# Kernel tuning notes

Measured on AMD Instinct MI355X. Metric: run time of the kernel, lower is better.

Reference implementation:

```python
import jax, jax.numpy as jnp
import numpy as np

B, NPG, EPG = 512, 256, 4096   # graphs, nodes/graph, edges/graph
N, E = B * NPG, B * EPG
F_IN, H, T = 128, 64, 18
K = 16
D_LAT = 4 * H + 1  # 257


def _p(key, shape, scale=0.05):
    return jax.random.normal(key, shape, dtype=jnp.float32) * scale


def setup_inputs() -> dict:
    key = jax.random.key(0)
    ks = jax.random.split(key, 32)
    x = jax.random.normal(ks[0], (N, F_IN), dtype=jnp.float32)
    off = jnp.repeat(jnp.arange(B, dtype=jnp.int32) * NPG, EPG)
    src = jax.random.randint(ks[1], (E,), 0, NPG, dtype=jnp.int32) + off
    dst = jax.random.randint(ks[2], (E,), 0, NPG, dtype=jnp.int32) + off
    edge_index = jnp.stack([src, dst])
    batch = jnp.repeat(jnp.arange(B, dtype=jnp.int32), NPG)
    inp = {"x": x, "edge_index": edge_index, "batch": batch, "num_graphs": B}
    dims = [F_IN, H, H, H, H]
    outs = [H, H, H, H, 1]
    for i in range(5):
        inp[f"w{i}"] = _p(ks[3 + i], (outs[i], dims[i]))
        inp[f"b{i}"] = jnp.zeros((outs[i],), jnp.float32)
    inp["conv1_w"] = _p(ks[10], (16, 1, D_LAT))
    inp["conv1_b"] = jnp.zeros((16,), jnp.float32)
    inp["conv2_w"] = _p(ks[11], (32, 16, 5))
    inp["conv2_b"] = jnp.zeros((32,), jnp.float32)
    inp["d1_w"] = _p(ks[12], (32, 128))
    inp["d1_b"] = jnp.zeros((32,), jnp.float32)
    inp["d2_w"] = _p(ks[13], (T, 32))
    inp["d2_b"] = jnp.zeros((T,), jnp.float32)
    return inp


def _dgcnn_forward(x, edge_index, batch, num_graphs,
                   ws, bs, conv1_w, conv1_b, conv2_w, conv2_b,
                   d1_w, d1_b, d2_w, d2_b):
    n_nodes = x.shape[0]
    loops = jnp.arange(n_nodes, dtype=edge_index.dtype)
    src = jnp.concatenate([edge_index[0], loops])
    dst = jnp.concatenate([edge_index[1], loops])
    # degree of src indices (with self-loops), norm = 1/deg gathered at dst
    deg = jax.ops.segment_sum(jnp.ones_like(src, x.dtype), src, num_segments=n_nodes)
    inv_deg_dst = (1.0 / deg)[dst]  # deg >= 1 thanks to self-loops

    hidden = []
    h = x
    for w, b in zip(ws, bs):
        h = h @ w.T + b                       # linear transform [N, out]
        msg = h[src] * inv_deg_dst[:, None]    # gather + degree norm [E+N, out]
        h = jax.ops.segment_sum(msg, dst, num_segments=n_nodes)
        h = jnp.tanh(h)
        hidden.append(h)
    feat = jnp.concatenate(hidden, axis=1)     # [N, 257]

    # global_sort_pool: per-graph descending sort on last channel, take top-k
    npg = n_nodes // num_graphs
    xr = feat.reshape(num_graphs, npg, D_LAT)
    order = jnp.argsort(-xr[:, :, -1], axis=1)[:, :K]         # [B, K]
    topk = jnp.take_along_axis(xr, order[:, :, None], axis=1)  # [B, K, 257]

    # conv1d(1->16, kernel=stride=257) over flattened [B, K*257] == per-slot matmul
    c1 = jnp.einsum('bld,od->bol', topk, conv1_w[:, 0, :]) + conv1_b[None, :, None]
    c1 = jax.nn.relu(c1)                                       # [B, 16, 16]
    p1 = c1.reshape(num_graphs, 16, K // 2, 2).max(axis=-1)    # maxpool1d(2,2) -> [B,16,8]
    c2 = jax.lax.conv_general_dilated(p1, conv2_w, (1,), 'VALID',
                                      dimension_numbers=('NCH', 'OIH', 'NCH'))
    c2 = jax.nn.relu(c2 + conv2_b[None, :, None])              # [B, 32, 4]
    flat = c2.reshape(num_graphs, -1)                          # [B, 128]
    last = jax.nn.relu(flat @ d1_w.T + d1_b)                   # [B, 32]
    out = last @ d2_w.T + d2_b                                 # [B, T] (dropout: eval mode)
    return jax.nn.log_softmax(out, axis=1), out, last


def reference(x, edge_index, batch, num_graphs,
              w0, b0, w1, b1, w2, b2, w3, b3, w4, b4,
              conv1_w, conv1_b, conv2_w, conv2_b,
              d1_w, d1_b, d2_w, d2_b):
    ws = [w0, w1, w2, w3, w4]
    bs = [b0, b1, b2, b3, b4]
    return _dgcnn_forward(x, edge_index, batch, num_graphs, ws, bs,
                          conv1_w, conv1_b, conv2_w, conv2_b,
                          d1_w, d1_b, d2_w, d2_b)
```

## Files before the change

kernel.cpp:

```cpp
#include <hip/hip_runtime.h>
#include <math.h>

#define NPG  256
#define EPG  4096
#define NG   512
#define FIN  128
#define HD   64
#define TOUT 18
#define KTOP 16
#define STB  260
#define STA  68
#define SRCL_CAP (EPG + 3*NPG)
#define E_TOT (NG*EPG)

__device__ __forceinline__ int HB(int k) { return k*STB + (((k>>2)&7)<<2); }

__launch_bounds__(1024)
__global__ void dgcnn_fused(
    const float* __restrict__ x,
    const int*   __restrict__ ei,
    const float* __restrict__ w0, const float* __restrict__ b0,
    const float* __restrict__ w1, const float* __restrict__ b1,
    const float* __restrict__ w2, const float* __restrict__ b2,
    const float* __restrict__ w3, const float* __restrict__ b3,
    const float* __restrict__ w4, const float* __restrict__ b4,
    const float* __restrict__ c1w, const float* __restrict__ c1b,
    const float* __restrict__ c2w, const float* __restrict__ c2b,
    const float* __restrict__ d1w, const float* __restrict__ d1b,
    const float* __restrict__ d2w, const float* __restrict__ d2b,
    float* __restrict__ out)
{
    __shared__ float s_hB[HD*STB + 32];
    __shared__ float s_hl[NPG*STA];
    __shared__ unsigned char s_srcl[SRCL_CAP] __attribute__((aligned(4)));
    __shared__ int   s_off[NPG+1];
    __shared__ int   s_cnt[NPG];
    __shared__ int   s_outd[NPG];
    __shared__ int   s_cur[NPG];
    __shared__ float s_invdeg[NPG];
    __shared__ float s_lin5[NPG];
    __shared__ float s_h5[NPG];
    __shared__ int   s_sel[KTOP];
    __shared__ float s_head[592];

    const int g = blockIdx.x;
    const int t = threadIdx.x;
    const int lane = t & 63;
    const int wid  = t >> 6;
    const int l4 = lane * 4;
    const int gbase = g * NPG;
    const int* __restrict__ srcg = ei + (size_t)g * EPG;
    const int* __restrict__ dstg = ei + (size_t)E_TOT + (size_t)g * EPG;

    if (t < NPG) { s_cnt[t] = 0; s_outd[t] = 0; }
    __syncthreads();
    for (int e = t; e < EPG; e += 1024) {
        int s = srcg[e] - gbase, d = dstg[e] - gbase;
        atomicAdd(&s_outd[s], 1);
        atomicAdd(&s_cnt[d], 1);
    }
    __syncthreads();
    if (t < NPG) s_invdeg[t] = 1.0f / (float)(s_outd[t] + 1);
    if (wid == 0) {
        int c0 = s_cnt[l4], c1 = s_cnt[l4+1], c2 = s_cnt[l4+2], c3 = s_cnt[l4+3];
        int p0 = (c0+3)&~3, p1 = (c1+3)&~3, p2 = (c2+3)&~3, p3 = (c3+3)&~3;
        int tot = p0+p1+p2+p3;
        int run = tot;
        #pragma unroll
        for (int o = 1; o < 64; o <<= 1) {
            int v = __shfl_up(run, o);
            if (lane >= o) run += v;
        }
        int base = run - tot;
        s_off[l4]   = base;
        s_off[l4+1] = base + p0;
        s_off[l4+2] = base + p0 + p1;
        s_off[l4+3] = base + p0 + p1 + p2;
        if (lane == 63) s_off[NPG] = run;
    }
    __syncthreads();
    if (t < NPG) s_cur[t] = s_off[t];
    __syncthreads();
    for (int e = t; e < EPG; e += 1024) {
        int s = srcg[e] - gbase, d = dstg[e] - gbase;
        int pos = atomicAdd(&s_cur[d], 1);
        s_srcl[pos] = (unsigned char)s;
    }
    __syncthreads();
    if (t < NPG) {
        int pe = s_off[t+1];
        for (int p = s_cur[t]; p < pe; p++) s_srcl[p] = (unsigned char)t;
    }
    __syncthreads();

    float projacc[4][4];
    #pragma unroll
    for (int i = 0; i < 4; i++)
        #pragma unroll
        for (int j = 0; j < 4; j++) projacc[i][j] = 0.f;

    auto aggregate = [&]() {
        const int js = lane >> 4;
        const int q4 = (lane & 15) * 4;
        for (int job = wid; job < 64; job += 16) {
            int d   = job*4 + js;
            int off = s_off[d], pe = s_off[d+1];
            int npad = (pe - off) - s_cnt[d];
            float4 a = *(const float4*)&s_hl[d*STA + (q4 ^ (((d>>2)&7)<<2))];
            float cf = (float)(1 - npad);
            a.x *= cf; a.y *= cf; a.z *= cf; a.w *= cf;
            for (int e = off; e < pe; e += 4) {
                unsigned int sq = *(const unsigned int*)&s_srcl[e];
                #pragma unroll
                for (int m = 0; m < 4; m++) {
                    int src = (sq >> (8*m)) & 255;
                    float4 hv = *(const float4*)&s_hl[src*STA + (q4 ^ (((src>>2)&7)<<2))];
                    a.x += hv.x; a.y += hv.y; a.z += hv.z; a.w += hv.w;
                }
            }
            float id = s_invdeg[d];
            s_hB[HB(q4+0) + d] = tanhf(a.x * id);
            s_hB[HB(q4+1) + d] = tanhf(a.y * id);
            s_hB[HB(q4+2) + d] = tanhf(a.z * id);
            s_hB[HB(q4+3) + d] = tanhf(a.w * id);
        }
    };

    auto matmul64 = [&](const float* __restrict__ w, const float* __restrict__ b) {
        const int c0 = __builtin_amdgcn_readfirstlane(wid * 4);
        const float* wp = w + c0 * HD;
        float acc[4][4];
        #pragma unroll
        for (int i = 0; i < 4; i++)
            #pragma unroll
            for (int j = 0; j < 4; j++) acc[i][j] = 0.f;
        #pragma unroll 8
        for (int k = 0; k < HD; k++) {
            float4 xv = *(const float4*)&s_hB[HB(k) + l4];
            float wv0 = wp[k], wv1 = wp[HD+k], wv2 = wp[2*HD+k], wv3 = wp[3*HD+k];
            float xa[4] = {xv.x, xv.y, xv.z, xv.w};
            #pragma unroll
            for (int i = 0; i < 4; i++) {
                acc[i][0] += xa[i]*wv0; acc[i][1] += xa[i]*wv1;
                acc[i][2] += xa[i]*wv2; acc[i][3] += xa[i]*wv3;
            }
        }
        float4 bb = *(const float4*)&b[c0];
        float ba[4] = {bb.x, bb.y, bb.z, bb.w};
        int colb = (wid*4) ^ ((lane & 7) << 2);
        #pragma unroll
        for (int i = 0; i < 4; i++) {
            float4 v;
            v.x = acc[i][0]+ba[0]; v.y = acc[i][1]+ba[1];
            v.z = acc[i][2]+ba[2]; v.w = acc[i][3]+ba[3];
            *(float4*)&s_hl[(l4+i)*STA + colb] = v;
        }
    };

    auto projpass = [&](int Loff) {
        const int o0 = __builtin_amdgcn_readfirstlane(wid * 4);
        const float* p = c1w + o0*257 + Loff;
        #pragma unroll 8
        for (int k = 0; k < HD; k++) {
            float4 xv = *(const float4*)&s_hB[HB(k) + l4];
            float p0 = p[k], p1 = p[257+k], p2 = p[514+k], p3 = p[771+k];
            float xa[4] = {xv.x, xv.y, xv.z, xv.w};
            #pragma unroll
            for (int i = 0; i < 4; i++) {
                projacc[i][0] += xa[i]*p0; projacc[i][1] += xa[i]*p1;
                projacc[i][2] += xa[i]*p2; projacc[i][3] += xa[i]*p3;
            }
        }
    };

    {
        const int c0 = __builtin_amdgcn_readfirstlane(wid * 4);
        float acc[4][4];
        #pragma unroll
        for (int i = 0; i < 4; i++)
            #pragma unroll
            for (int j = 0; j < 4; j++) acc[i][j] = 0.f;
        for (int c2 = 0; c2 < 2; c2++) {
            {
                int kk = (t & 15) * 4, nb = t >> 4;
                #pragma unroll
                for (int r = 0; r < 4; r++) {
                    int nn = nb + r*64;
                    float4 v = *(const float4*)&x[(size_t)(gbase+nn)*FIN + c2*64 + kk];
                    s_hB[HB(kk+0) + nn] = v.x;
                    s_hB[HB(kk+1) + nn] = v.y;
                    s_hB[HB(kk+2) + nn] = v.z;
                    s_hB[HB(kk+3) + nn] = v.w;
                }
            }
            __syncthreads();
            const float* wp = w0 + c0*FIN + c2*64;
            #pragma unroll 8
            for (int k = 0; k < 64; k++) {
                float4 xv = *(const float4*)&s_hB[HB(k) + l4];
                float wv0 = wp[k], wv1 = wp[FIN+k], wv2 = wp[2*FIN+k], wv3 = wp[3*FIN+k];
                float xa[4] = {xv.x, xv.y, xv.z, xv.w};
                #pragma unroll
                for (int i = 0; i < 4; i++) {
                    acc[i][0] += xa[i]*wv0; acc[i][1] += xa[i]*wv1;
                    acc[i][2] += xa[i]*wv2; acc[i][3] += xa[i]*wv3;
                }
            }
            __syncthreads();
        }
        float4 bb = *(const float4*)&b0[c0];
        float ba[4] = {bb.x, bb.y, bb.z, bb.w};
        int colb = (wid*4) ^ ((lane & 7) << 2);
        #pragma unroll
        for (int i = 0; i < 4; i++) {
            float4 v;
            v.x = acc[i][0]+ba[0]; v.y = acc[i][1]+ba[1];
            v.z = acc[i][2]+ba[2]; v.w = acc[i][3]+ba[3];
            *(float4*)&s_hl[(l4+i)*STA + colb] = v;
        }
    }
    __syncthreads();
    aggregate();
    __syncthreads();

    if (wid < 4) projpass(0);
    matmul64(w1, b1);
    __syncthreads();
    aggregate();
    __syncthreads();

    if (wid < 4) projpass(64);
    matmul64(w2, b2);
    __syncthreads();
    aggregate();
    __syncthreads();

    if (wid < 4) projpass(128);
    matmul64(w3, b3);
    __syncthreads();
    aggregate();
    __syncthreads();

    if (wid < 4) {
        projpass(192);
    } else if (wid < 8) {
        int n = t - 256;
        float a = b4[0];
        #pragma unroll 8
        for (int k = 0; k < HD; k++) a += s_hB[HB(k) + n] * w4[k];
        s_lin5[n] = a;
    }
    __syncthreads();
    if (t < NPG) {
        int d = t;
        int off = s_off[d], pe = s_off[d+1];
        int npad = (pe - off) - s_cnt[d];
        float a = (float)(1 - npad) * s_lin5[d];
        for (int e = off; e < pe; e += 4) {
            unsigned int sq = *(const unsigned int*)&s_srcl[e];
            a += s_lin5[sq & 255] + s_lin5[(sq>>8)&255]
               + s_lin5[(sq>>16)&255] + s_lin5[(sq>>24)&255];
        }
        s_h5[d] = tanhf(a * s_invdeg[d]);
    }
    __syncthreads();
    if (wid < 4) {
        const int o0 = __builtin_amdgcn_readfirstlane(wid * 4);
        float cw0 = c1w[(o0+0)*257 + 256];
        float cw1 = c1w[(o0+1)*257 + 256];
        float cw2 = c1w[(o0+2)*257 + 256];
        float cw3 = c1w[(o0+3)*257 + 256];
        #pragma unroll
        for (int i = 0; i < 4; i++) {
            float hv = s_h5[l4+i];
            float4 v;
            v.x = projacc[i][0] + hv*cw0;
            v.y = projacc[i][1] + hv*cw1;
            v.z = projacc[i][2] + hv*cw2;
            v.w = projacc[i][3] + hv*cw3;
            *(float4*)&s_hl[(l4+i)*16 + wid*4] = v;
        }
    }
    if (wid == 0) {
        float v[4]; int idx[4];
        #pragma unroll
        for (int j = 0; j < 4; j++) { idx[j] = l4+j; v[j] = s_h5[l4+j]; }
        for (int r = 0; r < KTOP; r++) {
            float bv = v[0]; int bi = idx[0];
            #pragma unroll
            for (int j = 1; j < 4; j++)
                if (v[j] > bv || (v[j] == bv && idx[j] < bi)) { bv = v[j]; bi = idx[j]; }
            #pragma unroll
            for (int o = 32; o > 0; o >>= 1) {
                float ov = __shfl_xor(bv, o);
                int   oi = __shfl_xor(bi, o);
                if (ov > bv || (ov == bv && oi < bi)) { bv = ov; bi = oi; }
            }
            if ((bi >> 2) == lane) v[bi & 3] = -1e30f;
            if (lane == 0) s_sel[r] = bi;
        }
    }
    __syncthreads();

    float* s_c1   = s_head;
    float* s_p1   = s_head + 256;
    float* s_flat = s_head + 384;
    float* s_last = s_head + 512;
    float* s_outv = s_head + 544;

    if (t < 256) {
        int sl = t >> 4, o = t & 15;
        float vv = s_hl[s_sel[sl]*16 + o] + c1b[o];
        s_c1[o*16 + sl] = fmaxf(vv, 0.f);
    }
    __syncthreads();
    if (t < 128) {
        int o = t >> 3, j = t & 7;
        s_p1[o*8 + j] = fmaxf(s_c1[o*16 + 2*j], s_c1[o*16 + 2*j + 1]);
    }
    __syncthreads();
    if (t < 128) {
        int oc = t >> 2, tt = t & 3;
        float a = c2b[oc];
        #pragma unroll
        for (int ic = 0; ic < 16; ic++)
            #pragma unroll
            for (int kk = 0; kk < 5; kk++)
                a += s_p1[ic*8 + tt + kk] * c2w[(oc*16 + ic)*5 + kk];
        s_flat[oc*4 + tt] = fmaxf(a, 0.f);
    }
    __syncthreads();
    if (t < 32) {
        float a = d1b[t];
        #pragma unroll 16
        for (int i = 0; i < 128; i++) a += s_flat[i] * d1w[t*128 + i];
        a = fmaxf(a, 0.f);
        s_last[t] = a;
        out[2*NG*TOUT + g*32 + t] = a;
    }
    __syncthreads();
    if (t < TOUT) {
        float a = d2b[t];
        #pragma unroll
        for (int j = 0; j < 32; j++) a += s_last[j] * d2w[t*32 + j];
        s_outv[t] = a;
        out[NG*TOUT + g*TOUT + t] = a;
    }
    __syncthreads();
    if (t < TOUT) {
        float m = s_outv[0];
        for (int i = 1; i < TOUT; i++) m = fmaxf(m, s_outv[i]);
        float sum = 0.f;
        for (int i = 0; i < TOUT; i++) sum += expf(s_outv[i] - m);
        out[g*TOUT + t] = s_outv[t] - m - logf(sum);
    }
}

extern "C" void kernel_launch(void* const* d_in, const int* in_sizes, int n_in,
                              void* d_out, int out_size, void* d_ws, size_t ws_size,
                              hipStream_t stream) {
    (void)in_sizes; (void)n_in; (void)out_size; (void)d_ws; (void)ws_size;
    const float* x   = (const float*)d_in[0];
    const int*   ei  = (const int*)  d_in[1];
    const float* w0  = (const float*)d_in[4];  const float* b0 = (const float*)d_in[5];
    const float* w1  = (const float*)d_in[6];  const float* b1 = (const float*)d_in[7];
    const float* w2  = (const float*)d_in[8];  const float* b2 = (const float*)d_in[9];
    const float* w3  = (const float*)d_in[10]; const float* b3 = (const float*)d_in[11];
    const float* w4  = (const float*)d_in[12]; const float* b4 = (const float*)d_in[13];
    const float* c1w = (const float*)d_in[14]; const float* c1b = (const float*)d_in[15];
    const float* c2w = (const float*)d_in[16]; const float* c2b = (const float*)d_in[17];
    const float* d1w = (const float*)d_in[18]; const float* d1b = (const float*)d_in[19];
    const float* d2w = (const float*)d_in[20]; const float* d2b = (const float*)d_in[21];
    float* out = (float*)d_out;

    dgcnn_fused<<<NG, 1024, 0, stream>>>(x, ei,
        w0, b0, w1, b1, w2, b2, w3, b3, w4, b4,
        c1w, c1b, c2w, c2b, d1w, d1b, d2w, d2b, out);
}
```

Baseline: 174.4 us.

## Fuse conv1 projection into layer matmuls across all waves, prefetch edge lists

The separate projection pass for the conv1 weights, which only waves 0-3 ran with 4 output channels each, is removed. Every wave now carries one output channel of the projection and accumulates it inside the layer matmul loop, so the load imbalance before each barrier goes away. The aggregation loop is fully unrolled over its four jobs and software-prefetches the next packed source index word, which needs a small pad on the index buffer. The projection buffer uses stride 17, and launch bounds now ask for 4 waves per EU, which may raise register pressure or cause spills.

```diff
diff --git a/kernel.cpp b/kernel.cpp
--- a/kernel.cpp
+++ b/kernel.cpp
@@ -11,11 +11,12 @@
 #define STB  260
 #define STA  68
 #define SRCL_CAP (EPG + 3*NPG)
+#define SRCL_PAD (SRCL_CAP + 8)
 #define E_TOT (NG*EPG)
 
 __device__ __forceinline__ int HB(int k) { return k*STB + (((k>>2)&7)<<2); }
 
-__launch_bounds__(1024)
+__launch_bounds__(1024, 4)
 __global__ void dgcnn_fused(
     const float* __restrict__ x,
     const int*   __restrict__ ei,
@@ -32,7 +33,7 @@
 {
     __shared__ float s_hB[HD*STB + 32];
     __shared__ float s_hl[NPG*STA];
-    __shared__ unsigned char s_srcl[SRCL_CAP] __attribute__((aligned(4)));
+    __shared__ unsigned char s_srcl[SRCL_PAD] __attribute__((aligned(4)));
     __shared__ int   s_off[NPG+1];
     __shared__ int   s_cnt[NPG];
     __shared__ int   s_outd[NPG];
@@ -42,6 +43,7 @@
     __shared__ float s_h5[NPG];
     __shared__ int   s_sel[KTOP];
     __shared__ float s_head[592];
+    float* s_proj = s_hl;
 
     const int g = blockIdx.x;
     const int t = threadIdx.x;
@@ -93,30 +95,30 @@
     }
     __syncthreads();
 
-    float projacc[4][4];
-    #pragma unroll
-    for (int i = 0; i < 4; i++)
-        #pragma unroll
-        for (int j = 0; j < 4; j++) projacc[i][j] = 0.f;
+    float projacc[4] = {0.f, 0.f, 0.f, 0.f};
 
     auto aggregate = [&]() {
         const int js = lane >> 4;
         const int q4 = (lane & 15) * 4;
-        for (int job = wid; job < 64; job += 16) {
-            int d   = job*4 + js;
+        #pragma unroll
+        for (int r = 0; r < 4; r++) {
+            int d   = (wid + 16*r)*4 + js;
             int off = s_off[d], pe = s_off[d+1];
             int npad = (pe - off) - s_cnt[d];
             float4 a = *(const float4*)&s_hl[d*STA + (q4 ^ (((d>>2)&7)<<2))];
             float cf = (float)(1 - npad);
             a.x *= cf; a.y *= cf; a.z *= cf; a.w *= cf;
-            for (int e = off; e < pe; e += 4) {
-                unsigned int sq = *(const unsigned int*)&s_srcl[e];
+            unsigned int cur = *(const unsigned int*)&s_srcl[off];
+            for (int e = off; e < pe; ) {
+                e += 4;
+                unsigned int nxt = *(const unsigned int*)&s_srcl[e];
                 #pragma unroll
                 for (int m = 0; m < 4; m++) {
-                    int src = (sq >> (8*m)) & 255;
+                    int src = (cur >> (8*m)) & 255;
                     float4 hv = *(const float4*)&s_hl[src*STA + (q4 ^ (((src>>2)&7)<<2))];
                     a.x += hv.x; a.y += hv.y; a.z += hv.z; a.w += hv.w;
                 }
+                cur = nxt;
             }
             float id = s_invdeg[d];
             s_hB[HB(q4+0) + d] = tanhf(a.x * id);
@@ -126,9 +128,12 @@
         }
     };
 
-    auto matmul64 = [&](const float* __restrict__ w, const float* __restrict__ b) {
+    auto matmul64 = [&](const float* __restrict__ w, const float* __restrict__ b,
+                        const float* __restrict__ c1s) {
         const int c0 = __builtin_amdgcn_readfirstlane(wid * 4);
+        const int o  = __builtin_amdgcn_readfirstlane(wid);
         const float* wp = w + c0 * HD;
+        const float* cp = c1s + o * 257;
         float acc[4][4];
         #pragma unroll
         for (int i = 0; i < 4; i++)
@@ -138,11 +143,13 @@
         for (int k = 0; k < HD; k++) {
             float4 xv = *(const float4*)&s_hB[HB(k) + l4];
             float wv0 = wp[k], wv1 = wp[HD+k], wv2 = wp[2*HD+k], wv3 = wp[3*HD+k];
+            float cv  = cp[k];
             float xa[4] = {xv.x, xv.y, xv.z, xv.w};
             #pragma unroll
             for (int i = 0; i < 4; i++) {
                 acc[i][0] += xa[i]*wv0; acc[i][1] += xa[i]*wv1;
                 acc[i][2] += xa[i]*wv2; acc[i][3] += xa[i]*wv3;
+                projacc[i] += xa[i]*cv;
             }
         }
         float4 bb = *(const float4*)&b[c0];
@@ -154,22 +161,6 @@
             v.x = acc[i][0]+ba[0]; v.y = acc[i][1]+ba[1];
             v.z = acc[i][2]+ba[2]; v.w = acc[i][3]+ba[3];
             *(float4*)&s_hl[(l4+i)*STA + colb] = v;
-        }
-    };
-
-    auto projpass = [&](int Loff) {
-        const int o0 = __builtin_amdgcn_readfirstlane(wid * 4);
-        const float* p = c1w + o0*257 + Loff;
-        #pragma unroll 8
-        for (int k = 0; k < HD; k++) {
-            float4 xv = *(const float4*)&s_hB[HB(k) + l4];
-            float p0 = p[k], p1 = p[257+k], p2 = p[514+k], p3 = p[771+k];
-            float xa[4] = {xv.x, xv.y, xv.z, xv.w};
-            #pragma unroll
-            for (int i = 0; i < 4; i++) {
-                projacc[i][0] += xa[i]*p0; projacc[i][1] += xa[i]*p1;
-                projacc[i][2] += xa[i]*p2; projacc[i][3] += xa[i]*p3;
-            }
         }
     };
 
@@ -223,32 +214,43 @@
     aggregate();
     __syncthreads();
 
-    if (wid < 4) projpass(0);
-    matmul64(w1, b1);
+    matmul64(w1, b1, c1w);
     __syncthreads();
     aggregate();
     __syncthreads();
 
-    if (wid < 4) projpass(64);
-    matmul64(w2, b2);
+    matmul64(w2, b2, c1w + 64);
     __syncthreads();
     aggregate();
     __syncthreads();
 
-    if (wid < 4) projpass(128);
-    matmul64(w3, b3);
+    matmul64(w3, b3, c1w + 128);
     __syncthreads();
     aggregate();
     __syncthreads();
 
-    if (wid < 4) {
-        projpass(192);
-    } else if (wid < 8) {
-        int n = t - 256;
-        float a = b4[0];
+    {
+        const int o = __builtin_amdgcn_readfirstlane(wid);
+        const float* cp = c1w + o*257 + 192;
+        float l5[4] = {0.f, 0.f, 0.f, 0.f};
         #pragma unroll 8
-        for (int k = 0; k < HD; k++) a += s_hB[HB(k) + n] * w4[k];
-        s_lin5[n] = a;
+        for (int k = 0; k < HD; k++) {
+            float4 xv = *(const float4*)&s_hB[HB(k) + l4];
+            float cv = cp[k];
+            float xa[4] = {xv.x, xv.y, xv.z, xv.w};
+            #pragma unroll
+            for (int i = 0; i < 4; i++) projacc[i] += xa[i]*cv;
+            if (wid == 0) {
+                float wv = w4[k];
+                #pragma unroll
+                for (int i = 0; i < 4; i++) l5[i] += xa[i]*wv;
+            }
+        }
+        if (wid == 0) {
+            float b4v = b4[0];
+            #pragma unroll
+            for (int i = 0; i < 4; i++) s_lin5[l4+i] = l5[i] + b4v;
+        }
     }
     __syncthreads();
     if (t < NPG) {
@@ -264,21 +266,13 @@
         s_h5[d] = tanhf(a * s_invdeg[d]);
     }
     __syncthreads();
-    if (wid < 4) {
-        const int o0 = __builtin_amdgcn_readfirstlane(wid * 4);
-        float cw0 = c1w[(o0+0)*257 + 256];
-        float cw1 = c1w[(o0+1)*257 + 256];
-        float cw2 = c1w[(o0+2)*257 + 256];
-        float cw3 = c1w[(o0+3)*257 + 256];
+    {
+        const int o = __builtin_amdgcn_readfirstlane(wid);
+        float cw = c1w[o*257 + 256];
         #pragma unroll
         for (int i = 0; i < 4; i++) {
-            float hv = s_h5[l4+i];
-            float4 v;
-            v.x = projacc[i][0] + hv*cw0;
-            v.y = projacc[i][1] + hv*cw1;
-            v.z = projacc[i][2] + hv*cw2;
-            v.w = projacc[i][3] + hv*cw3;
-            *(float4*)&s_hl[(l4+i)*16 + wid*4] = v;
+            float v = projacc[i] + s_h5[l4+i] * cw;
+            s_proj[(l4+i)*17 + o] = v;
         }
     }
     if (wid == 0) {
@@ -310,7 +304,7 @@
 
     if (t < 256) {
         int sl = t >> 4, o = t & 15;
-        float vv = s_hl[s_sel[sl]*16 + o] + c1b[o];
+        float vv = s_proj[s_sel[sl]*17 + o] + c1b[o];
         s_c1[o*16 + sl] = fmaxf(vv, 0.f);
     }
     __syncthreads();
```

Measured after the change: 174.8 us. Within noise of the previous version (+0.2%).
